# Kernel optimization log

Measured on AMD Instinct MI355X. Metric: run time of the kernel, lower is better.

Reference implementation:

```python
import jax, jax.numpy as jnp
import numpy as np

DECAY = 0.99
EPS = 1e-05


def setup_inputs() -> dict:
    key = jax.random.key(0)
    k1, k2 = jax.random.split(key)
    B, C, H, W = 16, 64, 32, 32
    K = 8192
    z_e = jax.random.normal(k1, (B, C, H, W), dtype=jnp.float32)
    embedding = jax.random.normal(k2, (K, C), dtype=jnp.float32)
    cluster_size = jnp.zeros((K,), dtype=jnp.float32)
    embedding_avg = embedding  # initialized as a clone of the codebook
    return {"z_e": z_e, "embedding": embedding, "cluster_size": cluster_size,
            "embedding_avg": embedding_avg}


def reference(z_e, embedding, cluster_size, embedding_avg):
    B, C, H, W = z_e.shape
    K = embedding.shape[0]
    # [N, C] tokens
    z_flat = jnp.transpose(z_e, (0, 2, 3, 1)).reshape(-1, C)
    d = ((z_flat * z_flat).sum(-1, keepdims=True)
         - 2.0 * (z_flat @ embedding.T)
         + (embedding * embedding).sum(-1))
    indices = jnp.argmin(d, axis=1)  # [N] int
    z_q_flat = embedding[indices]    # [N, C]
    z_q = jnp.transpose(z_q_flat.reshape(B, H, W, C), (0, 3, 1, 2))
    # EMA codebook update (training path); one-hot matmuls expressed as segment sums
    counts = jax.ops.segment_sum(jnp.ones(z_flat.shape[0], dtype=z_flat.dtype),
                                 indices, num_segments=K)            # encodings.sum(0)
    dw = jax.ops.segment_sum(z_flat, indices, num_segments=K)        # encodings.T @ z_flat
    new_cluster_size = DECAY * cluster_size + (1.0 - DECAY) * counts
    new_embedding_avg = DECAY * embedding_avg + (1.0 - DECAY) * dw
    n = new_cluster_size.sum()
    cs = (new_cluster_size + EPS) / (n + K * EPS) * n
    new_embedding = new_embedding_avg / cs[:, None]
    # straight-through estimator
    z_q_st = z_e + jax.lax.stop_gradient(z_q - z_e)
    return (z_q_st, indices.reshape(B, H * W), z_q,
            new_embedding, new_cluster_size, new_embedding_avg)
```

## Files before the change

kernel.cpp:

```cpp
#include <hip/hip_runtime.h>

#define DECAYF 0.99f
#define OMDF   0.01f
#define TAU    3.5e-2f

typedef unsigned int u32;
typedef unsigned long long u64;
typedef __attribute__((ext_vector_type(8))) _Float16 f16x8;
typedef __attribute__((ext_vector_type(4))) float f32x4;

#define EN_OFF     0
#define EFRAG_OFF  32768
#define IDX_OFF    32768
#define LIST_OFF   98304
#define BEST1_OFF  2129920
#define BEST2_OFF  3178496
#define CNT_OFF    3702784

__device__ __forceinline__ u64 enc_pair(float s, int idx) {
  u32 u = __float_as_uint(s);
  u = (u & 0x80000000u) ? ~u : (u | 0x80000000u);
  return ((u64)u << 32) | (u32)(~idx);
}
__device__ __forceinline__ float dec_score(u64 e) {
  u32 u = (u32)(e >> 32);
  u = (u & 0x80000000u) ? (u & 0x7fffffffu) : ~u;
  return __uint_as_float(u);
}
__device__ __forceinline__ int dec_idx(u64 e) { return (int)(~(u32)e); }
__device__ __forceinline__ unsigned short f2h(float f) {
  union { _Float16 h; unsigned short u; } v;
  v.h = (_Float16)f;
  return v.u;
}
__device__ __forceinline__ float exact_dot(const float* __restrict__ sx,
                                           const float* __restrict__ emb, int k) {
  const float4* e = (const float4*)(emb + (size_t)k * 64);
  float a = 0.f;
#pragma unroll
  for (int q = 0; q < 16; ++q) {
    float4 v = e[q];
    a = fmaf(sx[4 * q],     v.x, a);
    a = fmaf(sx[4 * q + 1], v.y, a);
    a = fmaf(sx[4 * q + 2], v.z, a);
    a = fmaf(sx[4 * q + 3], v.w, a);
  }
  return a;
}

__global__ __launch_bounds__(256) void k_prep(const float* __restrict__ emb,
                                              const float* __restrict__ cs_in,
                                              const float* __restrict__ avg_in,
                                              const float* __restrict__ z_e,
                                              float* __restrict__ en,
                                              unsigned char* __restrict__ efrag,
                                              unsigned char* __restrict__ zfrag,
                                              float* __restrict__ out4,
                                              float* __restrict__ out5,
                                              int* __restrict__ cnt,
                                              float* __restrict__ nsum) {
  __shared__ float warr[4];
  int bid = blockIdx.x;
  if (bid < 512) {
    int tid = bid * 256 + threadIdx.x;
    if (tid == 0) *cnt = 0;
    int k = tid >> 4, q = tid & 15;
    float4 v = ((const float4*)emb)[tid];
    ushort4 hv;
    hv.x = f2h(v.x); hv.y = f2h(v.y); hv.z = f2h(v.z); hv.w = f2h(v.w);
    size_t off = (size_t)(k >> 4) * 2048 + (size_t)(q >> 3) * 1024
               + (size_t)((q >> 1) & 3) * 256 + (size_t)(k & 15) * 16
               + (size_t)(q & 1) * 8;
    *(ushort4*)(efrag + off) = hv;
    float s = v.x * v.x + v.y * v.y + v.z * v.z + v.w * v.w;
    s += __shfl_xor(s, 1, 16);
    s += __shfl_xor(s, 2, 16);
    s += __shfl_xor(s, 4, 16);
    s += __shfl_xor(s, 8, 16);
    if (q == 0) en[k] = 0.5f * s;
  } else if (bid < 1031) {
    int tid = (bid - 512) * 256 + threadIdx.x;
    if (tid < 131072) {
      float4 v = ((const float4*)avg_in)[tid];
      v.x *= DECAYF; v.y *= DECAYF; v.z *= DECAYF; v.w *= DECAYF;
      ((float4*)out5)[tid] = v;
    }
  } else if (bid == 1031) {
    int thr = threadIdx.x;
    float s = 0.f;
#pragma unroll
    for (int q = 0; q < 8; ++q) {
      int idx = q * 256 + thr;
      float4 v = ((const float4*)cs_in)[idx];
      v.x *= DECAYF; v.y *= DECAYF; v.z *= DECAYF; v.w *= DECAYF;
      ((float4*)out4)[idx] = v;
      s += v.x + v.y + v.z + v.w;
    }
    s += __shfl_xor(s, 1, 64);
    s += __shfl_xor(s, 2, 64);
    s += __shfl_xor(s, 4, 64);
    s += __shfl_xor(s, 8, 64);
    s += __shfl_xor(s, 16, 64);
    s += __shfl_xor(s, 32, 64);
    if ((thr & 63) == 0) warr[thr >> 6] = s;
    __syncthreads();
    if (thr == 0) *nsum = warr[0] + warr[1] + warr[2] + warr[3];
  } else {
    int id = (bid - 1032) * 256 + threadIdx.x;
    int n = id & 16383, k = id >> 14;
    int b = n >> 10, hw = n & 1023;
    const float* zr = z_e + ((size_t)b << 16) + ((size_t)(k * 8) << 10) + hw;
    unsigned short u[8];
#pragma unroll
    for (int j = 0; j < 8; ++j) u[j] = f2h(zr[(size_t)j << 10]);
    size_t off = (size_t)(n >> 4) * 2048 + (size_t)(k >> 2) * 1024
               + (size_t)(k & 3) * 256 + (size_t)(n & 15) * 16;
    *(ushort4*)(zfrag + off)     = make_ushort4(u[0], u[1], u[2], u[3]);
    *(ushort4*)(zfrag + off + 8) = make_ushort4(u[4], u[5], u[6], u[7]);
  }
}

__global__ __launch_bounds__(256) void k_argmin_mfma(
    const unsigned char* __restrict__ zfrag,
    const unsigned char* __restrict__ efrag,
    const float* __restrict__ en, u64* __restrict__ best1,
    float* __restrict__ best2) {
  alignas(16) __shared__ unsigned char sbuf[2][8192];
  __shared__ float sen[1024];
  const int tb = blockIdx.x >> 3;
  const int sl = blockIdx.x & 7;
  const int wave = threadIdx.x >> 6, lane = threadIdx.x & 63;
  const int col = lane & 15, g4 = lane >> 4;
  const int token0 = tb * 128 + wave * 32;
  const int scb = sl << 10;

  ((float4*)sen)[threadIdx.x] = ((const float4*)(en + scb))[threadIdx.x];

  f16x8 a[2][2];
  {
    const unsigned char* zb = zfrag + ((size_t)(tb * 8 + wave * 2)) * 2048
                            + (size_t)g4 * 256 + (size_t)col * 16;
    a[0][0] = *(const f16x8*)(zb);
    a[0][1] = *(const f16x8*)(zb + 1024);
    a[1][0] = *(const f16x8*)(zb + 2048);
    a[1][1] = *(const f16x8*)(zb + 3072);
  }
  float b1[8], b2[8];
#pragma unroll
  for (int r = 0; r < 8; ++r) { b1[r] = -3.0e38f; b2[r] = -3.0e38f; }

  const unsigned char* gbase0 = efrag + (size_t)scb * 128;
  auto stage = [&](int ib, int buf) {
    const unsigned char* g = gbase0 + (size_t)ib * 8192 + (size_t)wave * 2048;
#pragma unroll
    for (int it = 0; it < 2; ++it) {
      __builtin_amdgcn_global_load_lds(
          (const __attribute__((address_space(1))) u32*)(g + it * 1024 + lane * 16),
          (__attribute__((address_space(3))) u32*)(&sbuf[buf][wave * 2048 + it * 1024]),
          16, 0, 0);
    }
  };
  stage(0, 0);
  for (int ib = 0; ib < 16; ++ib) {
    __syncthreads();
    if (ib < 15) stage(ib + 1, (ib + 1) & 1);
    const unsigned char* sb0 = &sbuf[ib & 1][0];
#pragma unroll
    for (int ct = 0; ct < 4; ++ct) {
      const int t = ib * 4 + ct;
      const float negen = -sen[t * 16 + col];
      f16x8 bf0 = *(const f16x8*)(sb0 + ct * 2048 + lane * 16);
      f16x8 bf1 = *(const f16x8*)(sb0 + ct * 2048 + 1024 + lane * 16);
      f32x4 acc0, acc1;
#pragma unroll
      for (int r = 0; r < 4; ++r) { acc0[r] = negen; acc1[r] = negen; }
      acc0 = __builtin_amdgcn_mfma_f32_16x16x32_f16(a[0][0], bf0, acc0, 0, 0, 0);
      acc0 = __builtin_amdgcn_mfma_f32_16x16x32_f16(a[0][1], bf1, acc0, 0, 0, 0);
      acc1 = __builtin_amdgcn_mfma_f32_16x16x32_f16(a[1][0], bf0, acc1, 0, 0, 0);
      acc1 = __builtin_amdgcn_mfma_f32_16x16x32_f16(a[1][1], bf1, acc1, 0, 0, 0);
      const u32 emb6 = (u32)(63 - t);
#pragma unroll
      for (int r = 0; r < 4; ++r) {
        float f0 = __uint_as_float((__float_as_uint(acc0[r]) & 0xFFFFFFC0u) | emb6);
        b2[r] = __builtin_amdgcn_fmed3f(f0, b1[r], b2[r]);
        b1[r] = fmaxf(b1[r], f0);
        float f1 = __uint_as_float((__float_as_uint(acc1[r]) & 0xFFFFFFC0u) | emb6);
        b2[4 + r] = __builtin_amdgcn_fmed3f(f1, b1[4 + r], b2[4 + r]);
        b1[4 + r] = fmaxf(b1[4 + r], f1);
      }
    }
  }
  int mi[8];
#pragma unroll
  for (int r = 0; r < 8; ++r) mi[r] = col;
#pragma unroll
  for (int st = 1; st < 16; st <<= 1) {
#pragma unroll
    for (int r = 0; r < 8; ++r) {
      float ob1 = __shfl_xor(b1[r], st, 64);
      float ob2 = __shfl_xor(b2[r], st, 64);
      int omi = __shfl_xor(mi[r], st, 64);
      bool ogt = ob1 > b1[r];
      b2[r] = fmaxf(fminf(b1[r], ob1), fmaxf(b2[r], ob2));
      mi[r] = ogt ? omi : mi[r];
      b1[r] = fmaxf(b1[r], ob1);
    }
  }
  if (col == 0) {
#pragma unroll
    for (int r = 0; r < 8; ++r) {
      int tset = r >> 2, rr = r & 3;
      int token = token0 + tset * 16 + g4 * 4 + rr;
      int t = 63 - (int)(__float_as_uint(b1[r]) & 63u);
      int gcode = scb + t * 16 + mi[r];
      best1[(size_t)sl * 16384 + token] = enc_pair(b1[r], gcode);
      best2[(size_t)sl * 16384 + token] = b2[r];
    }
  }
}

__global__ __launch_bounds__(256) void k_resolve(const u64* __restrict__ best1,
                                                 const float* __restrict__ best2,
                                                 int* __restrict__ idxa,
                                                 int* __restrict__ list,
                                                 int* __restrict__ cnt) {
  int n = blockIdx.x * 256 + threadIdx.x;
  u64 e[8];
  float sp[8];
#pragma unroll
  for (int s = 0; s < 8; ++s) {
    e[s]  = best1[(size_t)s * 16384 + n];
    sp[s] = best2[(size_t)s * 16384 + n];
  }
  u64 top = e[0];
#pragma unroll
  for (int s = 1; s < 8; ++s) top = e[s] > top ? e[s] : top;
  float second = -3.0e38f;
#pragma unroll
  for (int s = 0; s < 8; ++s) second = fmaxf(second, sp[s]);
#pragma unroll
  for (int s = 0; s < 8; ++s)
    if (e[s] != top) second = fmaxf(second, dec_score(e[s]));
  idxa[n] = dec_idx(top);
  if (dec_score(top) - second < TAU) {
    int p = atomicAdd(cnt, 1);
    list[p] = n;
  }
}

__global__ __launch_bounds__(256) void k_fixup(const float* __restrict__ z_e,
                                               const float* __restrict__ emb,
                                               const float* __restrict__ en,
                                               const u64* __restrict__ best1,
                                               const float* __restrict__ best2,
                                               const int* __restrict__ list,
                                               const int* __restrict__ cnt,
                                               int* __restrict__ idxa) {
  __shared__ float sx[64];
  __shared__ u64 esh[8];
  __shared__ float b2sh[8];
  __shared__ int cand[8];
  __shared__ int fsl[8];
  __shared__ int ncand, nfsl;
  __shared__ u64 red;
  int count = *cnt;
  for (int i = blockIdx.x; i < count; i += gridDim.x) {
    int n = list[i];
    __syncthreads();
    if (threadIdx.x == 0) { ncand = 0; nfsl = 0; red = 0ull; }
    if (threadIdx.x < 8) {
      esh[threadIdx.x]  = best1[(size_t)threadIdx.x * 16384 + n];
      b2sh[threadIdx.x] = best2[(size_t)threadIdx.x * 16384 + n];
    }
    if (threadIdx.x < 64) {
      sx[threadIdx.x] = z_e[((size_t)(n >> 10) << 16)
                            + ((size_t)threadIdx.x << 10) + (n & 1023)];
    }
    __syncthreads();
    u64 top = esh[0];
#pragma unroll
    for (int s = 1; s < 8; ++s) top = esh[s] > top ? esh[s] : top;
    float theta = dec_score(top) - TAU;
    if (threadIdx.x < 8) {
      int s = threadIdx.x;
      if (dec_score(esh[s]) >= theta) {
        int p = atomicAdd(&ncand, 1);
        cand[p] = dec_idx(esh[s]);
      }
      if (b2sh[s] >= theta) {
        int p = atomicAdd(&nfsl, 1);
        fsl[p] = s;
      }
    }
    __syncthreads();
    u64 myb = 0ull;
    if (threadIdx.x < ncand) {
      int k = cand[threadIdx.x];
      float a = exact_dot(sx, emb, k) - en[k];
      myb = enc_pair(a, k);
    }
    int nf = nfsl;
    for (int f = 0; f < nf; ++f) {
      int s = fsl[f];
      int k0 = (s << 10) + threadIdx.x;
      float a0 = exact_dot(sx, emb, k0)       - en[k0];
      float a1 = exact_dot(sx, emb, k0 + 256) - en[k0 + 256];
      float a2 = exact_dot(sx, emb, k0 + 512) - en[k0 + 512];
      float a3 = exact_dot(sx, emb, k0 + 768) - en[k0 + 768];
      u64 m0 = enc_pair(a0, k0),       m1 = enc_pair(a1, k0 + 256);
      u64 m2 = enc_pair(a2, k0 + 512), m3 = enc_pair(a3, k0 + 768);
      u64 ma = m0 > m1 ? m0 : m1, mb = m2 > m3 ? m2 : m3;
      u64 mm = ma > mb ? ma : mb;
      myb = mm > myb ? mm : myb;
    }
    if (myb) atomicMax(&red, myb);
    __syncthreads();
    if (threadIdx.x == 0) idxa[n] = dec_idx(red);
  }
}

__global__ __launch_bounds__(256) void k_scatter(const float* __restrict__ z_e,
                                                 const int* __restrict__ idxa,
                                                 float* __restrict__ out4,
                                                 float* __restrict__ out5) {
  int tid = blockIdx.x * 256 + threadIdx.x;
  int n = tid >> 6, c = tid & 63;
  int idx = idxa[n];
  int b = n >> 10, hw = n & 1023;
  float x = z_e[((size_t)b << 16) + ((size_t)c << 10) + hw];
  atomicAdd(out5 + (size_t)idx * 64 + c, OMDF * x);
  if (c == 0) atomicAdd(out4 + idx, OMDF);
}

__global__ __launch_bounds__(256) void k_gather(const float* __restrict__ z_e,
                                                const float* __restrict__ emb,
                                                const int* __restrict__ idxa,
                                                float* __restrict__ out0,
                                                float* __restrict__ out1,
                                                float* __restrict__ out2) {
  int tid = blockIdx.x * 256 + threadIdx.x;
  int hw4 = tid & 255;
  int c   = (tid >> 8) & 63;
  int b   = tid >> 14;
  int n0  = (b << 10) + (hw4 << 2);
  size_t off = ((size_t)b << 16) + ((size_t)c << 10) + ((size_t)hw4 << 2);
  float4 z = *(const float4*)(z_e + off);
  int i0 = idxa[n0], i1 = idxa[n0 + 1], i2 = idxa[n0 + 2], i3 = idxa[n0 + 3];
  float4 q;
  q.x = emb[(size_t)i0 * 64 + c];
  q.y = emb[(size_t)i1 * 64 + c];
  q.z = emb[(size_t)i2 * 64 + c];
  q.w = emb[(size_t)i3 * 64 + c];
  float4 st;
  st.x = z.x + (q.x - z.x);
  st.y = z.y + (q.y - z.y);
  st.z = z.z + (q.z - z.z);
  st.w = z.w + (q.w - z.w);
  *(float4*)(out2 + off) = q;
  *(float4*)(out0 + off) = st;
  if (c == 0) {
    float4 f = make_float4((float)i0, (float)i1, (float)i2, (float)i3);
    *(float4*)(out1 + n0) = f;
  }
}

__global__ __launch_bounds__(256) void k_final(const float* __restrict__ out4,
                                               const float* __restrict__ out5,
                                               const float* __restrict__ nsum,
                                               float* __restrict__ out3) {
  int tid = blockIdx.x * 256 + threadIdx.x;
  int k = tid >> 4;
  double nn  = (double)*nsum + 163.84;
  double ncs = (double)out4[k];
  double cs  = (ncs + 1e-5) / (nn + 8192.0 * 1e-5) * nn;
  float inv  = (float)(1.0 / cs);
  float4 v = ((const float4*)out5)[tid];
  v.x *= inv; v.y *= inv; v.z *= inv; v.w *= inv;
  ((float4*)out3)[tid] = v;
}

extern "C" void kernel_launch(void* const* d_in, const int* in_sizes, int n_in,
                              void* d_out, int out_size, void* d_ws, size_t ws_size,
                              hipStream_t stream) {
  const float* z_e    = (const float*)d_in[0];
  const float* emb    = (const float*)d_in[1];
  const float* cs_in  = (const float*)d_in[2];
  const float* avg_in = (const float*)d_in[3];

  float* out  = (float*)d_out;
  float* out0 = out;
  float* out1 = out0 + 1048576;
  float* out2 = out1 + 16384;
  float* out3 = out2 + 1048576;
  float* out4 = out3 + 524288;
  float* out5 = out4 + 8192;

  char* ws = (char*)d_ws;
  float* en            = (float*)(ws + EN_OFF);
  unsigned char* efrag = (unsigned char*)(ws + EFRAG_OFF);
  u64* best1           = (u64*)(ws + BEST1_OFF);
  float* best2         = (float*)(ws + BEST2_OFF);
  int* idxa            = (int*)(ws + IDX_OFF);
  int* list            = (int*)(ws + LIST_OFF);
  int* cnt             = (int*)(ws + CNT_OFF);
  float* nsum          = (float*)(ws + CNT_OFF + 4);
  unsigned char* zfrag = (unsigned char*)out0;

  k_prep       <<<1544, 256, 0, stream>>>(emb, cs_in, avg_in, z_e, en, efrag,
                                          zfrag, out4, out5, cnt, nsum);
  k_argmin_mfma<<<1024, 256, 0, stream>>>(zfrag, efrag, en, best1, best2);
  k_resolve    <<<64,   256, 0, stream>>>(best1, best2, idxa, list, cnt);
  k_fixup      <<<1024, 256, 0, stream>>>(z_e, emb, en, best1, best2, list, cnt, idxa);
  k_scatter    <<<4096, 256, 0, stream>>>(z_e, idxa, out4, out5);
  k_gather     <<<1024, 256, 0, stream>>>(z_e, emb, idxa, out0, out1, out2);
  k_final      <<<512,  256, 0, stream>>>(out4, out5, nsum, out3);
}
```

Measured before the change: 148.9 us.

## Split codebook into 16 slices, fuse resolve/fixup, tile z transposes through LDS

The argmin kernel now covers 512-code slices across 2048 blocks, up from 1024-code slices across 1024 blocks, which doubles parallelism and halves each block's serial loop. The resolve and fixup kernels are merged into one per-64-token kernel that refines flagged tokens inside the block, dropping the global list, the counter and one launch. The z_e to fp16 fragment conversion and the scatter kernel both stage a 64x128 tile in shared memory so their global reads are coalesced float4 loads. The trade-offs are twice as many best1/best2 partials to reduce and a serial in-block fixup loop, which could stall blocks that hold many near-tie tokens.

```diff
diff --git a/kernel.cpp b/kernel.cpp
--- a/kernel.cpp
+++ b/kernel.cpp
@@ -12,10 +12,9 @@
 #define EN_OFF     0
 #define EFRAG_OFF  32768
 #define IDX_OFF    32768
-#define LIST_OFF   98304
 #define BEST1_OFF  2129920
-#define BEST2_OFF  3178496
-#define CNT_OFF    3702784
+#define BEST2_OFF  4227072
+#define CNT_OFF    5275648
 
 __device__ __forceinline__ u64 enc_pair(float s, int idx) {
   u32 u = __float_as_uint(s);
@@ -57,13 +56,13 @@
                                               unsigned char* __restrict__ zfrag,
                                               float* __restrict__ out4,
                                               float* __restrict__ out5,
-                                              int* __restrict__ cnt,
                                               float* __restrict__ nsum) {
   __shared__ float warr[4];
+  __shared__ float sx[64][129];
   int bid = blockIdx.x;
+  int t = threadIdx.x;
   if (bid < 512) {
-    int tid = bid * 256 + threadIdx.x;
-    if (tid == 0) *cnt = 0;
+    int tid = bid * 256 + t;
     int k = tid >> 4, q = tid & 15;
     float4 v = ((const float4*)emb)[tid];
     ushort4 hv;
@@ -79,18 +78,17 @@
     s += __shfl_xor(s, 8, 16);
     if (q == 0) en[k] = 0.5f * s;
   } else if (bid < 1031) {
-    int tid = (bid - 512) * 256 + threadIdx.x;
+    int tid = (bid - 512) * 256 + t;
     if (tid < 131072) {
       float4 v = ((const float4*)avg_in)[tid];
       v.x *= DECAYF; v.y *= DECAYF; v.z *= DECAYF; v.w *= DECAYF;
       ((float4*)out5)[tid] = v;
     }
   } else if (bid == 1031) {
-    int thr = threadIdx.x;
     float s = 0.f;
 #pragma unroll
     for (int q = 0; q < 8; ++q) {
-      int idx = q * 256 + thr;
+      int idx = q * 256 + t;
       float4 v = ((const float4*)cs_in)[idx];
       v.x *= DECAYF; v.y *= DECAYF; v.z *= DECAYF; v.w *= DECAYF;
       ((float4*)out4)[idx] = v;
@@ -102,21 +100,37 @@
     s += __shfl_xor(s, 8, 64);
     s += __shfl_xor(s, 16, 64);
     s += __shfl_xor(s, 32, 64);
-    if ((thr & 63) == 0) warr[thr >> 6] = s;
-    __syncthreads();
-    if (thr == 0) *nsum = warr[0] + warr[1] + warr[2] + warr[3];
+    if ((t & 63) == 0) warr[t >> 6] = s;
+    __syncthreads();
+    if (t == 0) *nsum = warr[0] + warr[1] + warr[2] + warr[3];
   } else {
-    int id = (bid - 1032) * 256 + threadIdx.x;
-    int n = id & 16383, k = id >> 14;
-    int b = n >> 10, hw = n & 1023;
-    const float* zr = z_e + ((size_t)b << 16) + ((size_t)(k * 8) << 10) + hw;
-    unsigned short u[8];
-#pragma unroll
-    for (int j = 0; j < 8; ++j) u[j] = f2h(zr[(size_t)j << 10]);
-    size_t off = (size_t)(n >> 4) * 2048 + (size_t)(k >> 2) * 1024
-               + (size_t)(k & 3) * 256 + (size_t)(n & 15) * 16;
-    *(ushort4*)(zfrag + off)     = make_ushort4(u[0], u[1], u[2], u[3]);
-    *(ushort4*)(zfrag + off + 8) = make_ushort4(u[4], u[5], u[6], u[7]);
+    int n0 = (bid - 1032) * 128;
+    int b = n0 >> 10, hwb = n0 & 1023;
+#pragma unroll
+    for (int r = 0; r < 8; ++r) {
+      int g = r * 256 + t;
+      int c = g >> 5, f4 = g & 31;
+      float4 v = *(const float4*)(z_e + ((size_t)b << 16) + ((size_t)c << 10)
+                                  + hwb + f4 * 4);
+      sx[c][f4 * 4 + 0] = v.x;
+      sx[c][f4 * 4 + 1] = v.y;
+      sx[c][f4 * 4 + 2] = v.z;
+      sx[c][f4 * 4 + 3] = v.w;
+    }
+    __syncthreads();
+#pragma unroll
+    for (int r = 0; r < 4; ++r) {
+      int id = r * 256 + t;
+      int nl = id & 127, k = id >> 7;
+      int n = n0 + nl;
+      unsigned short u[8];
+#pragma unroll
+      for (int j = 0; j < 8; ++j) u[j] = f2h(sx[k * 8 + j][nl]);
+      size_t off = (size_t)(n >> 4) * 2048 + (size_t)(k >> 2) * 1024
+                 + (size_t)(k & 3) * 256 + (size_t)(n & 15) * 16;
+      *(ushort4*)(zfrag + off)     = make_ushort4(u[0], u[1], u[2], u[3]);
+      *(ushort4*)(zfrag + off + 8) = make_ushort4(u[4], u[5], u[6], u[7]);
+    }
   }
 }
 
@@ -126,15 +140,16 @@
     const float* __restrict__ en, u64* __restrict__ best1,
     float* __restrict__ best2) {
   alignas(16) __shared__ unsigned char sbuf[2][8192];
-  __shared__ float sen[1024];
-  const int tb = blockIdx.x >> 3;
-  const int sl = blockIdx.x & 7;
+  __shared__ float sen[512];
+  const int tb = blockIdx.x >> 4;
+  const int sl = blockIdx.x & 15;
   const int wave = threadIdx.x >> 6, lane = threadIdx.x & 63;
   const int col = lane & 15, g4 = lane >> 4;
   const int token0 = tb * 128 + wave * 32;
-  const int scb = sl << 10;
-
-  ((float4*)sen)[threadIdx.x] = ((const float4*)(en + scb))[threadIdx.x];
+  const int scb = sl << 9;
+
+  if (threadIdx.x < 128)
+    ((float4*)sen)[threadIdx.x] = ((const float4*)(en + scb))[threadIdx.x];
 
   f16x8 a[2][2];
   {
@@ -161,9 +176,9 @@
     }
   };
   stage(0, 0);
-  for (int ib = 0; ib < 16; ++ib) {
-    __syncthreads();
-    if (ib < 15) stage(ib + 1, (ib + 1) & 1);
+  for (int ib = 0; ib < 8; ++ib) {
+    __syncthreads();
+    if (ib < 7) stage(ib + 1, (ib + 1) & 1);
     const unsigned char* sb0 = &sbuf[ib & 1][0];
 #pragma unroll
     for (int ct = 0; ct < 4; ++ct) {
@@ -209,8 +224,8 @@
   if (col == 0) {
 #pragma unroll
     for (int r = 0; r < 8; ++r) {
-      int tset = r >> 2, rr = r & 3;
-      int token = token0 + tset * 16 + g4 * 4 + rr;
+      int tt = r >> 2, rr = r & 3;
+      int token = token0 + tt * 16 + g4 * 4 + rr;
       int t = 63 - (int)(__float_as_uint(b1[r]) & 63u);
       int gcode = scb + t * 16 + mi[r];
       best1[(size_t)sl * 16384 + token] = enc_pair(b1[r], gcode);
@@ -219,103 +234,80 @@
   }
 }
 
-__global__ __launch_bounds__(256) void k_resolve(const u64* __restrict__ best1,
-                                                 const float* __restrict__ best2,
-                                                 int* __restrict__ idxa,
-                                                 int* __restrict__ list,
-                                                 int* __restrict__ cnt) {
-  int n = blockIdx.x * 256 + threadIdx.x;
-  u64 e[8];
-  float sp[8];
-#pragma unroll
-  for (int s = 0; s < 8; ++s) {
-    e[s]  = best1[(size_t)s * 16384 + n];
-    sp[s] = best2[(size_t)s * 16384 + n];
-  }
-  u64 top = e[0];
-#pragma unroll
-  for (int s = 1; s < 8; ++s) top = e[s] > top ? e[s] : top;
-  float second = -3.0e38f;
-#pragma unroll
-  for (int s = 0; s < 8; ++s) second = fmaxf(second, sp[s]);
-#pragma unroll
-  for (int s = 0; s < 8; ++s)
-    if (e[s] != top) second = fmaxf(second, dec_score(e[s]));
-  idxa[n] = dec_idx(top);
-  if (dec_score(top) - second < TAU) {
-    int p = atomicAdd(cnt, 1);
-    list[p] = n;
-  }
-}
-
-__global__ __launch_bounds__(256) void k_fixup(const float* __restrict__ z_e,
-                                               const float* __restrict__ emb,
-                                               const float* __restrict__ en,
-                                               const u64* __restrict__ best1,
-                                               const float* __restrict__ best2,
-                                               const int* __restrict__ list,
-                                               const int* __restrict__ cnt,
-                                               int* __restrict__ idxa) {
-  __shared__ float sx[64];
-  __shared__ u64 esh[8];
-  __shared__ float b2sh[8];
-  __shared__ int cand[8];
-  __shared__ int fsl[8];
-  __shared__ int ncand, nfsl;
+__global__ __launch_bounds__(256) void k_resfix(const float* __restrict__ z_e,
+                                                const float* __restrict__ emb,
+                                                const float* __restrict__ en,
+                                                const u64* __restrict__ best1,
+                                                const float* __restrict__ best2,
+                                                int* __restrict__ idxa) {
+  __shared__ float sxr[64];
+  __shared__ int flist[64];
+  __shared__ float fth[64];
+  __shared__ int nflag;
+  __shared__ u32 fmask;
   __shared__ u64 red;
-  int count = *cnt;
-  for (int i = blockIdx.x; i < count; i += gridDim.x) {
-    int n = list[i];
-    __syncthreads();
-    if (threadIdx.x == 0) { ncand = 0; nfsl = 0; red = 0ull; }
-    if (threadIdx.x < 8) {
-      esh[threadIdx.x]  = best1[(size_t)threadIdx.x * 16384 + n];
-      b2sh[threadIdx.x] = best2[(size_t)threadIdx.x * 16384 + n];
-    }
-    if (threadIdx.x < 64) {
-      sx[threadIdx.x] = z_e[((size_t)(n >> 10) << 16)
-                            + ((size_t)threadIdx.x << 10) + (n & 1023)];
-    }
-    __syncthreads();
-    u64 top = esh[0];
-#pragma unroll
-    for (int s = 1; s < 8; ++s) top = esh[s] > top ? esh[s] : top;
-    float theta = dec_score(top) - TAU;
-    if (threadIdx.x < 8) {
-      int s = threadIdx.x;
-      if (dec_score(esh[s]) >= theta) {
-        int p = atomicAdd(&ncand, 1);
-        cand[p] = dec_idx(esh[s]);
+  int t = threadIdx.x;
+  int n0 = blockIdx.x * 64;
+  if (t == 0) nflag = 0;
+  __syncthreads();
+  if (t < 64) {
+    int n = n0 + t;
+    u64 e[16];
+#pragma unroll
+    for (int s = 0; s < 16; ++s) e[s] = best1[(size_t)s * 16384 + n];
+    u64 top = e[0];
+#pragma unroll
+    for (int s = 1; s < 16; ++s) top = e[s] > top ? e[s] : top;
+    float second = -3.0e38f;
+#pragma unroll
+    for (int s = 0; s < 16; ++s)
+      second = fmaxf(second, best2[(size_t)s * 16384 + n]);
+#pragma unroll
+    for (int s = 0; s < 16; ++s)
+      if (e[s] != top) second = fmaxf(second, dec_score(e[s]));
+    idxa[n] = dec_idx(top);
+    if (dec_score(top) - second < TAU) {
+      int p = atomicAdd(&nflag, 1);
+      flist[p] = n;
+      fth[p] = dec_score(top);
+    }
+  }
+  __syncthreads();
+  int nf = nflag;
+  for (int i = 0; i < nf; ++i) {
+    int n = flist[i];
+    float theta = fth[i] - TAU;
+    if (t == 0) { fmask = 0; red = 0ull; }
+    if (t < 64) {
+      sxr[t] = z_e[((size_t)(n >> 10) << 16) + ((size_t)t << 10) + (n & 1023)];
+    }
+    __syncthreads();
+    u64 myb = 0ull;
+    if (t < 16) {
+      u64 es = best1[(size_t)t * 16384 + n];
+      if (best2[(size_t)t * 16384 + n] >= theta) atomicOr(&fmask, 1u << t);
+      if (dec_score(es) >= theta) {
+        int k = dec_idx(es);
+        float a = exact_dot(sxr, emb, k) - en[k];
+        myb = enc_pair(a, k);
       }
-      if (b2sh[s] >= theta) {
-        int p = atomicAdd(&nfsl, 1);
-        fsl[p] = s;
-      }
-    }
-    __syncthreads();
-    u64 myb = 0ull;
-    if (threadIdx.x < ncand) {
-      int k = cand[threadIdx.x];
-      float a = exact_dot(sx, emb, k) - en[k];
-      myb = enc_pair(a, k);
-    }
-    int nf = nfsl;
-    for (int f = 0; f < nf; ++f) {
-      int s = fsl[f];
-      int k0 = (s << 10) + threadIdx.x;
-      float a0 = exact_dot(sx, emb, k0)       - en[k0];
-      float a1 = exact_dot(sx, emb, k0 + 256) - en[k0 + 256];
-      float a2 = exact_dot(sx, emb, k0 + 512) - en[k0 + 512];
-      float a3 = exact_dot(sx, emb, k0 + 768) - en[k0 + 768];
-      u64 m0 = enc_pair(a0, k0),       m1 = enc_pair(a1, k0 + 256);
-      u64 m2 = enc_pair(a2, k0 + 512), m3 = enc_pair(a3, k0 + 768);
-      u64 ma = m0 > m1 ? m0 : m1, mb = m2 > m3 ? m2 : m3;
-      u64 mm = ma > mb ? ma : mb;
+    }
+    __syncthreads();
+    u32 fm = fmask;
+    while (fm) {
+      int s = __ffs(fm) - 1;
+      fm &= fm - 1;
+      int k0 = (s << 9) + t;
+      float a0 = exact_dot(sxr, emb, k0)       - en[k0];
+      float a1 = exact_dot(sxr, emb, k0 + 256) - en[k0 + 256];
+      u64 m0 = enc_pair(a0, k0), m1 = enc_pair(a1, k0 + 256);
+      u64 mm = m0 > m1 ? m0 : m1;
       myb = mm > myb ? mm : myb;
     }
     if (myb) atomicMax(&red, myb);
     __syncthreads();
-    if (threadIdx.x == 0) idxa[n] = dec_idx(red);
+    if (t == 0) idxa[n] = dec_idx(red);
+    __syncthreads();
   }
 }
 
@@ -323,13 +315,30 @@
                                                  const int* __restrict__ idxa,
                                                  float* __restrict__ out4,
                                                  float* __restrict__ out5) {
-  int tid = blockIdx.x * 256 + threadIdx.x;
-  int n = tid >> 6, c = tid & 63;
-  int idx = idxa[n];
-  int b = n >> 10, hw = n & 1023;
-  float x = z_e[((size_t)b << 16) + ((size_t)c << 10) + hw];
-  atomicAdd(out5 + (size_t)idx * 64 + c, OMDF * x);
-  if (c == 0) atomicAdd(out4 + idx, OMDF);
+  __shared__ float sx[64][129];
+  int t = threadIdx.x;
+  int n0 = blockIdx.x * 128;
+  int b = n0 >> 10, hwb = n0 & 1023;
+#pragma unroll
+  for (int r = 0; r < 8; ++r) {
+    int g = r * 256 + t;
+    int c = g >> 5, f4 = g & 31;
+    float4 v = *(const float4*)(z_e + ((size_t)b << 16) + ((size_t)c << 10)
+                                + hwb + f4 * 4);
+    sx[c][f4 * 4 + 0] = v.x;
+    sx[c][f4 * 4 + 1] = v.y;
+    sx[c][f4 * 4 + 2] = v.z;
+    sx[c][f4 * 4 + 3] = v.w;
+  }
+  __syncthreads();
+  int wave = t >> 6, lane = t & 63;
+#pragma unroll
+  for (int i = 0; i < 32; ++i) {
+    int tok = wave * 32 + i;
+    int idx = idxa[n0 + tok];
+    atomicAdd(out5 + (size_t)idx * 64 + lane, OMDF * sx[lane][tok]);
+    if (lane == 0) atomicAdd(out4 + idx, OMDF);
+  }
 }
 
 __global__ __launch_bounds__(256) void k_gather(const float* __restrict__ z_e,
@@ -401,17 +410,14 @@
   u64* best1           = (u64*)(ws + BEST1_OFF);
   float* best2         = (float*)(ws + BEST2_OFF);
   int* idxa            = (int*)(ws + IDX_OFF);
-  int* list            = (int*)(ws + LIST_OFF);
-  int* cnt             = (int*)(ws + CNT_OFF);
   float* nsum          = (float*)(ws + CNT_OFF + 4);
   unsigned char* zfrag = (unsigned char*)out0;
 
-  k_prep       <<<1544, 256, 0, stream>>>(emb, cs_in, avg_in, z_e, en, efrag,
-                                          zfrag, out4, out5, cnt, nsum);
-  k_argmin_mfma<<<1024, 256, 0, stream>>>(zfrag, efrag, en, best1, best2);
-  k_resolve    <<<64,   256, 0, stream>>>(best1, best2, idxa, list, cnt);
-  k_fixup      <<<1024, 256, 0, stream>>>(z_e, emb, en, best1, best2, list, cnt, idxa);
-  k_scatter    <<<4096, 256, 0, stream>>>(z_e, idxa, out4, out5);
+  k_prep       <<<1160, 256, 0, stream>>>(emb, cs_in, avg_in, z_e, en, efrag,
+                                          zfrag, out4, out5, nsum);
+  k_argmin_mfma<<<2048, 256, 0, stream>>>(zfrag, efrag, en, best1, best2);
+  k_resfix     <<<256,  256, 0, stream>>>(z_e, emb, en, best1, best2, idxa);
+  k_scatter    <<<128,  256, 0, stream>>>(z_e, idxa, out4, out5);
   k_gather     <<<1024, 256, 0, stream>>>(z_e, emb, idxa, out0, out1, out2);
   k_final      <<<512,  256, 0, stream>>>(out4, out5, nsum, out3);
 }
```

After: 151.5 us. About the same (+1.7%).
